# Performance work log

Hardware: AMD Instinct MI355X
Metric: run time of the kernel (lower is better)

Reference implementation:

```python
import jax, jax.numpy as jnp
import numpy as np

BUCKET_SIZE = 64
LOOK_BACKWARD = 1
LOOK_FORWARD = 0  # causal => no look forward
CAUSAL = True


def look_around(x, backward, forward, pad_value):
    # x: [b, buckets, bucket_size, ...]; pads along the bucket axis and concats
    # shifted windows along the intra-bucket axis (dim=2), matching torch look_around.
    t = x.shape[1]
    pad_cfg = ((0, 0), (backward, forward)) + ((0, 0),) * (x.ndim - 2)
    padded = jnp.pad(x, pad_cfg, constant_values=pad_value)
    return jnp.concatenate([padded[:, i:i + t] for i in range(forward + backward + 1)], axis=2)


def setup_inputs() -> dict:
    key = jax.random.key(0)
    kq, kk, kv = jax.random.split(key, 3)
    shape = (4, 16, 4096, 64)  # [batch, heads, seq, head_dim]
    q = jax.random.normal(kq, shape, dtype=jnp.float32)
    k = jax.random.normal(kk, shape, dtype=jnp.float32)
    v = jax.random.normal(kv, shape, dtype=jnp.float32)
    return {"q": q, "k": k, "v": v}


def reference(q, k, v):
    shape = q.shape
    # merge batch and heads
    merge = lambda t: t.reshape(-1, t.shape[-2], t.shape[-1])
    q, k, v = merge(q), merge(k), merge(v)
    b, t, e = q.shape
    assert t % BUCKET_SIZE == 0
    buckets = t // BUCKET_SIZE

    ticker = jnp.arange(t, dtype=jnp.int32)[None, :]          # [1, t]
    b_t = ticker.reshape(1, buckets, BUCKET_SIZE)              # [1, buckets, bucket]

    bucket_fn = lambda x: x.reshape(b, buckets, BUCKET_SIZE, e)
    bq, bk, bv = bucket_fn(q), bucket_fn(k), bucket_fn(v)

    bk = look_around(bk, LOOK_BACKWARD, LOOK_FORWARD, 0.0)
    bv = look_around(bv, LOOK_BACKWARD, LOOK_FORWARD, 0.0)
    bq_t = b_t                                                 # query positions
    bq_k = look_around(b_t, LOOK_BACKWARD, LOOK_FORWARD, -1)   # key positions, -1 = pad

    scale = e ** (-0.5)
    dots = jnp.einsum('bnie,bnje->bnij', bq, bk) * scale
    mask_value = -jnp.finfo(dots.dtype).max

    if CAUSAL:
        causal_mask = bq_t[:, :, :, None] < bq_k[:, :, None, :]
        dots = jnp.where(causal_mask, mask_value, dots)

    pad_mask = bq_k[:, :, None, :] == -1
    dots = jnp.where(pad_mask, mask_value, dots)

    attn = jax.nn.softmax(dots, axis=-1)
    out = jnp.einsum('bnij,bnje->bnie', attn, bv)
    return out.reshape(shape)
```

## Files before the change

### kernel.cpp

```cpp
#include <hip/hip_runtime.h>
#include <hip/hip_bf16.h>

typedef __attribute__((ext_vector_type(8))) __bf16 bf16x8;
typedef __attribute__((ext_vector_type(4))) float f32x4;

#define SEQ   4096
#define HDIM  64
#define BKT   64

__device__ __forceinline__ unsigned f2bf_u(float f) {
    unsigned u = __float_as_uint(f);
    u += 0x7FFFu + ((u >> 16) & 1u);
    return u >> 16;
}
__device__ __forceinline__ unsigned pk2(float a, float b) {
    return f2bf_u(a) | (f2bf_u(b) << 16);
}
__device__ __forceinline__ int swzV(int row) {
    return ((row & 7) ^ ((row >> 3) & 7)) << 4;
}

__global__ void __launch_bounds__(256, 4) local_attn_kernel(
    const float* __restrict__ q, const float* __restrict__ k,
    const float* __restrict__ v, float* __restrict__ out)
{
    __shared__ __align__(16) unsigned short sBuf[128 * 64];

    const int tid = threadIdx.x;
    const int bid0 = blockIdx.x;
    const int lg = (bid0 & 7) * 512 + (bid0 >> 3);
    const int bh = lg >> 6;
    const int bucket = lg & 63;

    const int qoff = (bh * SEQ + bucket * BKT) * HDIM;
    const int koff = qoff - BKT * HDIM;

    const int lane = tid & 63;
    const int wid  = tid >> 6;
    const int g = lane >> 4, m = lane & 15;
    const int g4 = g * 4;
    const int qbase = wid * 16;

    char* const sB = reinterpret_cast<char*>(sBuf);

    float4 kreg[8], qreg[4];
    #pragma unroll
    for (int i = 0; i < 8; ++i) {
        const int flat = i * 1024 + tid * 4;
        kreg[i] = make_float4(0.f, 0.f, 0.f, 0.f);
        if (bucket > 0 || i >= 4)
            kreg[i] = *reinterpret_cast<const float4*>(k + koff + flat);
    }
    #pragma unroll
    for (int h = 0; h < 2; ++h) {
        const float* qp = q + qoff + (qbase + m) * HDIM + h * 32 + g * 8;
        qreg[2 * h]     = *reinterpret_cast<const float4*>(qp);
        qreg[2 * h + 1] = *reinterpret_cast<const float4*>(qp + 4);
    }
    __builtin_amdgcn_sched_barrier(0);

    #pragma unroll
    for (int i = 0; i < 8; ++i) {
        const int flat = i * 1024 + tid * 4;
        const int row = flat >> 6, col = flat & 63;
        uint2 p;
        p.x = pk2(kreg[i].x, kreg[i].y);
        p.y = pk2(kreg[i].z, kreg[i].w);
        const int byte = (row * 128 + col * 2) ^ ((row & 7) << 4);
        *reinterpret_cast<uint2*>(sB + byte) = p;
    }
    const float scale = 0.125f * 1.44269504f;
    bf16x8 bq[2];
    #pragma unroll
    for (int h = 0; h < 2; ++h) {
        uint4 u;
        u.x = pk2(qreg[2 * h].x * scale, qreg[2 * h].y * scale);
        u.y = pk2(qreg[2 * h].z * scale, qreg[2 * h].w * scale);
        u.z = pk2(qreg[2 * h + 1].x * scale, qreg[2 * h + 1].y * scale);
        u.w = pk2(qreg[2 * h + 1].z * scale, qreg[2 * h + 1].w * scale);
        bq[h] = __builtin_bit_cast(bf16x8, u);
    }
    __syncthreads();

    f32x4 acc[8];
    #pragma unroll
    for (int c = 0; c < 8; ++c) acc[c] = (f32x4){0.f, 0.f, 0.f, 0.f};
    __builtin_amdgcn_s_setprio(1);
    #pragma unroll
    for (int c = 0; c < 8; ++c) {
        const int krow = c * 16 + m;
        #pragma unroll
        for (int h = 0; h < 2; ++h) {
            const int byte = (krow * 128 + h * 64 + g * 16) ^ ((m & 7) << 4);
            const bf16x8 ak = *reinterpret_cast<const bf16x8*>(sB + byte);
            acc[c] = __builtin_amdgcn_mfma_f32_16x16x32_bf16(ak, bq[h], acc[c], 0, 0, 0);
        }
    }
    __builtin_amdgcn_s_setprio(0);

    float4 vreg[8];
    #pragma unroll
    for (int i = 0; i < 8; ++i) {
        const int kb = i * 16 + wid * 4;
        vreg[i] = make_float4(0.f, 0.f, 0.f, 0.f);
        if (bucket > 0 || i >= 4)
            vreg[i] = *reinterpret_cast<const float4*>(v + koff + (kb + g) * HDIM + m * 4);
    }
    __builtin_amdgcn_sched_barrier(0);

    const int qb = qbase + m;
    float mx = -3e38f;
    #pragma unroll
    for (int c = 0; c < 8; ++c) {
        #pragma unroll
        for (int r = 0; r < 4; ++r) {
            const int kk = c * 16 + g4 + r;
            const bool dead = (c >= 4) ? (kk - 64 > qb) : (bucket == 0);
            const float s = dead ? -1e30f : acc[c][r];
            acc[c][r] = s;
            mx = fmaxf(mx, s);
        }
    }
    mx = fmaxf(mx, __shfl_xor(mx, 16));
    mx = fmaxf(mx, __shfl_xor(mx, 32));
    float sum = 0.f;
    uint2 pb[8];
    #pragma unroll
    for (int c = 0; c < 8; ++c) {
        const float p0 = __builtin_amdgcn_exp2f(acc[c][0] - mx);
        const float p1 = __builtin_amdgcn_exp2f(acc[c][1] - mx);
        const float p2 = __builtin_amdgcn_exp2f(acc[c][2] - mx);
        const float p3 = __builtin_amdgcn_exp2f(acc[c][3] - mx);
        sum += (p0 + p1) + (p2 + p3);
        pb[c].x = pk2(p0, p1);
        pb[c].y = pk2(p2, p3);
    }
    sum += __shfl_xor(sum, 16);
    sum += __shfl_xor(sum, 32);
    const float rl = 1.0f / sum;

    __syncthreads();

    #pragma unroll
    for (int i = 0; i < 8; ++i) {
        const int kb = i * 16 + wid * 4;
        const float4 f = vreg[i];
        const unsigned P0 = pk2(f.x, f.y);
        const unsigned P1 = pk2(f.z, f.w);
        const unsigned own  = (g < 2) ? P0 : P1;
        const unsigned send = (g < 2) ? P1 : P0;
        const unsigned R = __shfl_xor(send, 32);
        const unsigned T = __shfl_xor(own, 16);
        const unsigned U = __shfl_xor(R, 16);
        const unsigned A0 = (g < 2) ? own : R;
        const unsigned A1 = (g < 2) ? T : U;
        const unsigned A2 = (g < 2) ? R : own;
        const unsigned A3 = (g < 2) ? U : T;
        const int sdx = g & 1;
        const unsigned k0 = sdx ? A1 : A0, k1 = sdx ? A0 : A1;
        const unsigned k2 = sdx ? A3 : A2, k3 = sdx ? A2 : A3;
        const unsigned G0 = sdx ? ((k0 >> 16) | (k1 & 0xFFFF0000u)) : ((k0 & 0xFFFFu) | (k1 << 16));
        const unsigned G1 = sdx ? ((k2 >> 16) | (k3 & 0xFFFF0000u)) : ((k2 & 0xFFFFu) | (k3 << 16));
        const int er = m * 4 + g;
        const int byte = (er * 256 + kb * 2) ^ swzV(er);
        uint2 p; p.x = G0; p.y = G1;
        *reinterpret_cast<uint2*>(sB + byte) = p;
    }

    const int l0 = m + ((g & 1) << 5);
    const int l1 = l0 + 16;
    const bool hi2 = (g >> 1) != 0;
    bf16x8 bp[4];
    #pragma unroll
    for (int kt = 0; kt < 4; ++kt) {
        const unsigned a0x = __shfl(pb[2 * kt].x, l0),     a0y = __shfl(pb[2 * kt].y, l0);
        const unsigned a1x = __shfl(pb[2 * kt + 1].x, l0), a1y = __shfl(pb[2 * kt + 1].y, l0);
        const unsigned b0x = __shfl(pb[2 * kt].x, l1),     b0y = __shfl(pb[2 * kt].y, l1);
        const unsigned b1x = __shfl(pb[2 * kt + 1].x, l1), b1y = __shfl(pb[2 * kt + 1].y, l1);
        uint4 u;
        u.x = hi2 ? a1x : a0x;
        u.y = hi2 ? a1y : a0y;
        u.z = hi2 ? b1x : b0x;
        u.w = hi2 ? b1y : b0y;
        bp[kt] = __builtin_bit_cast(bf16x8, u);
    }
    __syncthreads();

    f32x4 oacc[4];
    #pragma unroll
    for (int et = 0; et < 4; ++et) oacc[et] = (f32x4){0.f, 0.f, 0.f, 0.f};
    __builtin_amdgcn_s_setprio(1);
    #pragma unroll
    for (int et = 0; et < 4; ++et) {
        const int row = et * 16 + m;
        #pragma unroll
        for (int kt = 0; kt < 4; ++kt) {
            const int byte = (row * 256 + kt * 64 + g * 16) ^ swzV(row);
            const bf16x8 av = *reinterpret_cast<const bf16x8*>(sB + byte);
            oacc[et] = __builtin_amdgcn_mfma_f32_16x16x32_bf16(av, bp[kt], oacc[et], 0, 0, 0);
        }
    }
    __builtin_amdgcn_s_setprio(0);

    const int qrow = qbase + m;
    #pragma unroll
    for (int et = 0; et < 4; ++et) {
        f32x4 o = oacc[et];
        o[0] *= rl; o[1] *= rl; o[2] *= rl; o[3] *= rl;
        *reinterpret_cast<float4*>(out + qoff + qrow * HDIM + et * 16 + g4) =
            *reinterpret_cast<float4*>(&o);
    }
}

extern "C" void kernel_launch(void* const* d_in, const int* in_sizes, int n_in,
                              void* d_out, int out_size, void* d_ws, size_t ws_size,
                              hipStream_t stream) {
    const float* q = (const float*)d_in[0];
    const float* k = (const float*)d_in[1];
    const float* v = (const float*)d_in[2];
    float* out = (float*)d_out;
    const int bh = in_sizes[0] / (SEQ * HDIM);
    const int nblocks = bh * (SEQ / BKT);
    hipLaunchKernelGGL(local_attn_kernel, dim3(nblocks), dim3(256), 0, stream,
                       q, k, v, out);
}
```

Measured before the change: 50.47 us.

## Issue K, V, Q loads together with separate LDS buffers and staged waitcnts

Splits the shared buffer into separate K and transposed-V regions so V no longer has to wait for QK^T to finish before being staged. All global loads are issued up front through inline asm and drained with staged vmcnt waits, and two barriers collapse into one. For bucket 0 the out-of-range K/V rows are redirected to valid memory instead of being zeroed, relying on the mask to discard them. This doubles LDS use per block, which may reduce occupancy, and raises register pressure.

```diff
diff --git a/kernel.cpp b/kernel.cpp
--- a/kernel.cpp
+++ b/kernel.cpp
@@ -24,7 +24,8 @@
     const float* __restrict__ q, const float* __restrict__ k,
     const float* __restrict__ v, float* __restrict__ out)
 {
-    __shared__ __align__(16) unsigned short sBuf[128 * 64];
+    __shared__ __align__(16) unsigned short sK[128 * 64];
+    __shared__ __align__(16) unsigned short sVt[64 * 128];
 
     const int tid = threadIdx.x;
     const int bid0 = blockIdx.x;
@@ -34,6 +35,7 @@
 
     const int qoff = (bh * SEQ + bucket * BKT) * HDIM;
     const int koff = qoff - BKT * HDIM;
+    const int fix0 = (bucket == 0) ? (BKT * HDIM) : 0;
 
     const int lane = tid & 63;
     const int wid  = tid >> 6;
@@ -41,112 +43,53 @@
     const int g4 = g * 4;
     const int qbase = wid * 16;
 
-    char* const sB = reinterpret_cast<char*>(sBuf);
-
-    float4 kreg[8], qreg[4];
-    #pragma unroll
-    for (int i = 0; i < 8; ++i) {
-        const int flat = i * 1024 + tid * 4;
-        kreg[i] = make_float4(0.f, 0.f, 0.f, 0.f);
-        if (bucket > 0 || i >= 4)
-            kreg[i] = *reinterpret_cast<const float4*>(k + koff + flat);
+    char* const sKb = reinterpret_cast<char*>(sK);
+    char* const sVb = reinterpret_cast<char*>(sVt);
+
+    f32x4 kreg[8], vreg[8], qreg[4];
+    #pragma unroll
+    for (int i = 0; i < 8; ++i) {
+        const float* p = k + koff + ((i < 4) ? fix0 : 0) + i * 1024 + tid * 4;
+        asm volatile("global_load_dwordx4 %0, %1, off"
+                     : "=v"(kreg[i]) : "v"(p) : "memory");
+    }
+    #pragma unroll
+    for (int i = 0; i < 8; ++i) {
+        const int kb = i * 16 + wid * 4;
+        const float* p = v + koff + ((i < 4) ? fix0 : 0) + (kb + g) * HDIM + m * 4;
+        asm volatile("global_load_dwordx4 %0, %1, off"
+                     : "=v"(vreg[i]) : "v"(p) : "memory");
     }
     #pragma unroll
     for (int h = 0; h < 2; ++h) {
         const float* qp = q + qoff + (qbase + m) * HDIM + h * 32 + g * 8;
-        qreg[2 * h]     = *reinterpret_cast<const float4*>(qp);
-        qreg[2 * h + 1] = *reinterpret_cast<const float4*>(qp + 4);
-    }
+        asm volatile("global_load_dwordx4 %0, %1, off"
+                     : "=v"(qreg[2 * h]) : "v"(qp) : "memory");
+        asm volatile("global_load_dwordx4 %0, %1, off"
+                     : "=v"(qreg[2 * h + 1]) : "v"(qp + 4) : "memory");
+    }
+
+    asm volatile("s_waitcnt vmcnt(12)" ::: "memory");
     __builtin_amdgcn_sched_barrier(0);
-
     #pragma unroll
     for (int i = 0; i < 8; ++i) {
         const int flat = i * 1024 + tid * 4;
         const int row = flat >> 6, col = flat & 63;
         uint2 p;
-        p.x = pk2(kreg[i].x, kreg[i].y);
-        p.y = pk2(kreg[i].z, kreg[i].w);
+        p.x = pk2(kreg[i][0], kreg[i][1]);
+        p.y = pk2(kreg[i][2], kreg[i][3]);
         const int byte = (row * 128 + col * 2) ^ ((row & 7) << 4);
-        *reinterpret_cast<uint2*>(sB + byte) = p;
-    }
-    const float scale = 0.125f * 1.44269504f;
-    bf16x8 bq[2];
-    #pragma unroll
-    for (int h = 0; h < 2; ++h) {
-        uint4 u;
-        u.x = pk2(qreg[2 * h].x * scale, qreg[2 * h].y * scale);
-        u.y = pk2(qreg[2 * h].z * scale, qreg[2 * h].w * scale);
-        u.z = pk2(qreg[2 * h + 1].x * scale, qreg[2 * h + 1].y * scale);
-        u.w = pk2(qreg[2 * h + 1].z * scale, qreg[2 * h + 1].w * scale);
-        bq[h] = __builtin_bit_cast(bf16x8, u);
-    }
-    __syncthreads();
-
-    f32x4 acc[8];
-    #pragma unroll
-    for (int c = 0; c < 8; ++c) acc[c] = (f32x4){0.f, 0.f, 0.f, 0.f};
-    __builtin_amdgcn_s_setprio(1);
-    #pragma unroll
-    for (int c = 0; c < 8; ++c) {
-        const int krow = c * 16 + m;
-        #pragma unroll
-        for (int h = 0; h < 2; ++h) {
-            const int byte = (krow * 128 + h * 64 + g * 16) ^ ((m & 7) << 4);
-            const bf16x8 ak = *reinterpret_cast<const bf16x8*>(sB + byte);
-            acc[c] = __builtin_amdgcn_mfma_f32_16x16x32_bf16(ak, bq[h], acc[c], 0, 0, 0);
-        }
-    }
-    __builtin_amdgcn_s_setprio(0);
-
-    float4 vreg[8];
+        *reinterpret_cast<uint2*>(sKb + byte) = p;
+    }
+
+    asm volatile("s_waitcnt vmcnt(4)" ::: "memory");
+    __builtin_amdgcn_sched_barrier(0);
     #pragma unroll
     for (int i = 0; i < 8; ++i) {
         const int kb = i * 16 + wid * 4;
-        vreg[i] = make_float4(0.f, 0.f, 0.f, 0.f);
-        if (bucket > 0 || i >= 4)
-            vreg[i] = *reinterpret_cast<const float4*>(v + koff + (kb + g) * HDIM + m * 4);
-    }
-    __builtin_amdgcn_sched_barrier(0);
-
-    const int qb = qbase + m;
-    float mx = -3e38f;
-    #pragma unroll
-    for (int c = 0; c < 8; ++c) {
-        #pragma unroll
-        for (int r = 0; r < 4; ++r) {
-            const int kk = c * 16 + g4 + r;
-            const bool dead = (c >= 4) ? (kk - 64 > qb) : (bucket == 0);
-            const float s = dead ? -1e30f : acc[c][r];
-            acc[c][r] = s;
-            mx = fmaxf(mx, s);
-        }
-    }
-    mx = fmaxf(mx, __shfl_xor(mx, 16));
-    mx = fmaxf(mx, __shfl_xor(mx, 32));
-    float sum = 0.f;
-    uint2 pb[8];
-    #pragma unroll
-    for (int c = 0; c < 8; ++c) {
-        const float p0 = __builtin_amdgcn_exp2f(acc[c][0] - mx);
-        const float p1 = __builtin_amdgcn_exp2f(acc[c][1] - mx);
-        const float p2 = __builtin_amdgcn_exp2f(acc[c][2] - mx);
-        const float p3 = __builtin_amdgcn_exp2f(acc[c][3] - mx);
-        sum += (p0 + p1) + (p2 + p3);
-        pb[c].x = pk2(p0, p1);
-        pb[c].y = pk2(p2, p3);
-    }
-    sum += __shfl_xor(sum, 16);
-    sum += __shfl_xor(sum, 32);
-    const float rl = 1.0f / sum;
-
-    __syncthreads();
-
-    #pragma unroll
-    for (int i = 0; i < 8; ++i) {
-        const int kb = i * 16 + wid * 4;
-        const float4 f = vreg[i];
-        const unsigned P0 = pk2(f.x, f.y);
-        const unsigned P1 = pk2(f.z, f.w);
+        const f32x4 f = vreg[i];
+        const unsigned P0 = pk2(f[0], f[1]);
+        const unsigned P1 = pk2(f[2], f[3]);
         const unsigned own  = (g < 2) ? P0 : P1;
         const unsigned send = (g < 2) ? P1 : P0;
         const unsigned R = __shfl_xor(send, 32);
@@ -164,8 +107,70 @@
         const int er = m * 4 + g;
         const int byte = (er * 256 + kb * 2) ^ swzV(er);
         uint2 p; p.x = G0; p.y = G1;
-        *reinterpret_cast<uint2*>(sB + byte) = p;
-    }
+        *reinterpret_cast<uint2*>(sVb + byte) = p;
+    }
+
+    asm volatile("s_waitcnt vmcnt(0)" ::: "memory");
+    __builtin_amdgcn_sched_barrier(0);
+    const float scale = 0.125f * 1.44269504f;
+    bf16x8 bq[2];
+    #pragma unroll
+    for (int h = 0; h < 2; ++h) {
+        uint4 u;
+        u.x = pk2(qreg[2 * h][0] * scale, qreg[2 * h][1] * scale);
+        u.y = pk2(qreg[2 * h][2] * scale, qreg[2 * h][3] * scale);
+        u.z = pk2(qreg[2 * h + 1][0] * scale, qreg[2 * h + 1][1] * scale);
+        u.w = pk2(qreg[2 * h + 1][2] * scale, qreg[2 * h + 1][3] * scale);
+        bq[h] = __builtin_bit_cast(bf16x8, u);
+    }
+    __syncthreads();
+
+    f32x4 acc[8];
+    #pragma unroll
+    for (int c = 0; c < 8; ++c) acc[c] = (f32x4){0.f, 0.f, 0.f, 0.f};
+    __builtin_amdgcn_s_setprio(1);
+    #pragma unroll
+    for (int c = 0; c < 8; ++c) {
+        const int krow = c * 16 + m;
+        #pragma unroll
+        for (int h = 0; h < 2; ++h) {
+            const int byte = (krow * 128 + h * 64 + g * 16) ^ ((m & 7) << 4);
+            const bf16x8 ak = *reinterpret_cast<const bf16x8*>(sKb + byte);
+            acc[c] = __builtin_amdgcn_mfma_f32_16x16x32_bf16(ak, bq[h], acc[c], 0, 0, 0);
+        }
+    }
+    __builtin_amdgcn_s_setprio(0);
+
+    const int qb = qbase + m;
+    float mx = -3e38f;
+    #pragma unroll
+    for (int c = 0; c < 8; ++c) {
+        #pragma unroll
+        for (int r = 0; r < 4; ++r) {
+            const int kk = c * 16 + g4 + r;
+            const bool dead = (c >= 4) ? (kk - 64 > qb) : (bucket == 0);
+            const float s = dead ? -1e30f : acc[c][r];
+            acc[c][r] = s;
+            mx = fmaxf(mx, s);
+        }
+    }
+    mx = fmaxf(mx, __shfl_xor(mx, 16));
+    mx = fmaxf(mx, __shfl_xor(mx, 32));
+    float sum = 0.f;
+    uint2 pb[8];
+    #pragma unroll
+    for (int c = 0; c < 8; ++c) {
+        const float p0 = __builtin_amdgcn_exp2f(acc[c][0] - mx);
+        const float p1 = __builtin_amdgcn_exp2f(acc[c][1] - mx);
+        const float p2 = __builtin_amdgcn_exp2f(acc[c][2] - mx);
+        const float p3 = __builtin_amdgcn_exp2f(acc[c][3] - mx);
+        sum += (p0 + p1) + (p2 + p3);
+        pb[c].x = pk2(p0, p1);
+        pb[c].y = pk2(p2, p3);
+    }
+    sum += __shfl_xor(sum, 16);
+    sum += __shfl_xor(sum, 32);
+    const float rl = 1.0f / sum;
 
     const int l0 = m + ((g & 1) << 5);
     const int l1 = l0 + 16;
@@ -184,7 +189,6 @@
         u.w = hi2 ? b1y : b0y;
         bp[kt] = __builtin_bit_cast(bf16x8, u);
     }
-    __syncthreads();
 
     f32x4 oacc[4];
     #pragma unroll
@@ -196,7 +200,7 @@
         #pragma unroll
         for (int kt = 0; kt < 4; ++kt) {
             const int byte = (row * 256 + kt * 64 + g * 16) ^ swzV(row);
-            const bf16x8 av = *reinterpret_cast<const bf16x8*>(sB + byte);
+            const bf16x8 av = *reinterpret_cast<const bf16x8*>(sVb + byte);
             oacc[et] = __builtin_amdgcn_mfma_f32_16x16x32_bf16(av, bp[kt], oacc[et], 0, 0, 0);
         }
     }
```

New measurement: 46.04 us. 1.1x faster.
